# Optimization experiments

Measured on AMD Instinct MI355X. Metric: run time of the kernel, lower is better.

## Reference

```python
import math
import jax, jax.numpy as jnp
import numpy as np

NUM_HEADS = 16
QUERY_SIZE = 1024
SEQ = 2048
HEAD = QUERY_SIZE // NUM_HEADS  # qk_size = vo_size = 64


def setup_inputs() -> dict:
    key = jax.random.key(0)
    ks = jax.random.split(key, 8)
    s = 0.02
    query = jax.random.normal(ks[0], (SEQ, QUERY_SIZE), jnp.float32)
    key_ = jax.random.normal(ks[1], (SEQ, QUERY_SIZE), jnp.float32)
    value = jax.random.normal(ks[2], (SEQ, QUERY_SIZE), jnp.float32)
    # causal mask (mask='causal' with state=None -> offset 0)
    mask = jnp.tril(jnp.ones((SEQ, SEQ), dtype=bool))
    Wq = jax.random.normal(ks[3], (QUERY_SIZE, QUERY_SIZE), jnp.float32) * s
    Wk = jax.random.normal(ks[4], (QUERY_SIZE, QUERY_SIZE), jnp.float32) * s
    Wv = jax.random.normal(ks[5], (QUERY_SIZE, QUERY_SIZE), jnp.float32) * s
    Wo = jax.random.normal(ks[6], (QUERY_SIZE, QUERY_SIZE), jnp.float32) * s
    return {"query": query, "key_": key_, "value": value, "mask": mask,
            "Wq": Wq, "Wk": Wk, "Wv": Wv, "Wo": Wo}


def reference(query, key_, value, mask, Wq, Wk, Wv, Wo):
    H, D = NUMS = NUM_HEADS, HEAD
    S = query.shape[0]
    inv_sqrt_d = 1.0 / math.sqrt(D)
    # per-token linear projections, split into heads: [S, H, D]
    q = (query @ Wq.T).reshape(S, H, D)
    k = (key_ @ Wk.T).reshape(S, H, D)
    v = (value @ Wv.T).reshape(S, H, D)
    # NOTE: original divides BOTH q and k by sqrt(d) (effective 1/d scaling)
    q = q * inv_sqrt_d
    k = k * inv_sqrt_d
    # logits per head: [H, S, S]
    logits = jnp.einsum('shd,Shd->hsS', q, k)
    logits = jnp.where(mask[None, :, :], logits, jnp.finfo(logits.dtype).min)
    # per-head GLOBAL max subtraction, softmax in fp32, cast back (faithful)
    m = jnp.max(logits, axis=(1, 2), keepdims=True)
    weights = jax.nn.softmax((logits - m).astype(jnp.float32), axis=-1).astype(query.dtype)
    attn = jnp.einsum('hsS,ShD->shD', weights, v).reshape(S, H * D)
    return attn @ Wo.T
```

## Files before the change

### kernel.cpp

```cpp
#include <hip/hip_runtime.h>
#include <hip/hip_bf16.h>

typedef __bf16 bf16_t;
typedef __bf16 bf16x8 __attribute__((ext_vector_type(8)));
typedef float f32x4 __attribute__((ext_vector_type(4)));

#define MFMA(A, B, C) __builtin_amdgcn_mfma_f32_16x16x32_bf16(A, B, C, 0, 0, 0)

__global__ __launch_bounds__(256) void cvt_all(
    const float* __restrict__ q, const float* __restrict__ k, const float* __restrict__ v,
    const float* __restrict__ wq, const float* __restrict__ wk,
    const float* __restrict__ wv, const float* __restrict__ wo,
    bf16_t* __restrict__ xq, bf16_t* __restrict__ xk, bf16_t* __restrict__ xv,
    bf16_t* __restrict__ ywq, bf16_t* __restrict__ ywk,
    bf16_t* __restrict__ ywv, bf16_t* __restrict__ ywo)
{
  const long gid = (long)blockIdx.x * 256 + threadIdx.x;
  const float* s; bf16_t* d; long off; float sc = 1.0f;
  if (gid < 262144)       { s = q;  d = xq;  off = gid; }
  else if (gid < 524288)  { s = k;  d = xk;  off = gid - 262144; }
  else if (gid < 786432)  { s = v;  d = xv;  off = gid - 524288; }
  else if (gid < 917504)  { s = wq; d = ywq; off = gid - 786432;  sc = 0.125f; }
  else if (gid < 1048576) { s = wk; d = ywk; off = gid - 917504;  sc = 0.125f; }
  else if (gid < 1179648) { s = wv; d = ywv; off = gid - 1048576; }
  else                    { s = wo; d = ywo; off = gid - 1179648; }
  const float* p = s + off * 8;
  float4 a = *(const float4*)p, b = *(const float4*)(p + 4);
  bf16x8 o;
  o[0] = (bf16_t)(a.x * sc); o[1] = (bf16_t)(a.y * sc);
  o[2] = (bf16_t)(a.z * sc); o[3] = (bf16_t)(a.w * sc);
  o[4] = (bf16_t)(b.x * sc); o[5] = (bf16_t)(b.y * sc);
  o[6] = (bf16_t)(b.z * sc); o[7] = (bf16_t)(b.w * sc);
  *(bf16x8*)(d + off * 8) = o;
}

__device__ __forceinline__ void gemm_core(const bf16_t* __restrict__ A,
                                          const bf16_t* __restrict__ W,
                                          int bm, int bn,
                                          bf16_t* As, bf16_t* Bs,
                                          f32x4 (&acc)[4][2])
{
  const int tid = threadIdx.x, lane = tid & 63, wave = tid >> 6;
  const int l15 = lane & 15, l4 = lane >> 4;
  const int wm = (wave >> 1) * 64, wn = (wave & 1) * 32;

  bf16x8 ra[4], rb[2];
#pragma unroll
  for (int i = 0; i < 4; ++i) {
    int id = tid + 256 * i, row = id >> 3, c = id & 7;
    ra[i] = *(const bf16x8*)(A + (size_t)(bm + row) * 1024 + c * 8);
  }
#pragma unroll
  for (int i = 0; i < 2; ++i) {
    int id = tid + 256 * i, row = id >> 3, c = id & 7;
    rb[i] = *(const bf16x8*)(W + (size_t)(bn + row) * 1024 + c * 8);
  }

#pragma unroll
  for (int s = 0; s < 16; ++s) {
    __syncthreads();
#pragma unroll
    for (int i = 0; i < 4; ++i) {
      int id = tid + 256 * i, row = id >> 3, c = id & 7;
      *(bf16x8*)(&As[row * 64 + 8 * (c ^ (row & 7))]) = ra[i];
    }
#pragma unroll
    for (int i = 0; i < 2; ++i) {
      int id = tid + 256 * i, row = id >> 3, c = id & 7;
      *(bf16x8*)(&Bs[row * 64 + 8 * (c ^ (row & 7))]) = rb[i];
    }
    __syncthreads();
    if (s + 1 < 16) {
      const int k0 = (s + 1) * 64;
#pragma unroll
      for (int i = 0; i < 4; ++i) {
        int id = tid + 256 * i, row = id >> 3, c = id & 7;
        ra[i] = *(const bf16x8*)(A + (size_t)(bm + row) * 1024 + k0 + c * 8);
      }
#pragma unroll
      for (int i = 0; i < 2; ++i) {
        int id = tid + 256 * i, row = id >> 3, c = id & 7;
        rb[i] = *(const bf16x8*)(W + (size_t)(bn + row) * 1024 + k0 + c * 8);
      }
    }
#pragma unroll
    for (int ks = 0; ks < 2; ++ks) {
      bf16x8 af[4], bfr[2];
#pragma unroll
      for (int i = 0; i < 4; ++i)
        af[i] = *(const bf16x8*)(&As[(wm + i * 16 + l15) * 64 + 8 * ((ks * 4 + l4) ^ (l15 & 7))]);
#pragma unroll
      for (int j = 0; j < 2; ++j)
        bfr[j] = *(const bf16x8*)(&Bs[(wn + j * 16 + l15) * 64 + 8 * ((ks * 4 + l4) ^ (l15 & 7))]);
#pragma unroll
      for (int i = 0; i < 4; ++i)
#pragma unroll
        for (int j = 0; j < 2; ++j)
          acc[i][j] = MFMA(af[i], bfr[j], acc[i][j]);
    }
  }
}

__global__ __launch_bounds__(256) void gemm_qkv(
    const bf16_t* __restrict__ xq, const bf16_t* __restrict__ xk, const bf16_t* __restrict__ xv,
    const bf16_t* __restrict__ ywq, const bf16_t* __restrict__ ywk, const bf16_t* __restrict__ ywv,
    bf16_t* __restrict__ qo, bf16_t* __restrict__ ko, bf16_t* __restrict__ vt)
{
  __shared__ __align__(16) bf16_t As[128 * 64];
  __shared__ __align__(16) bf16_t Bs[64 * 64];
  const int z = blockIdx.z;
  const bf16_t* A = z == 0 ? xq : z == 1 ? xk : xv;
  const bf16_t* W = z == 0 ? ywq : z == 1 ? ywk : ywv;
  const int bm = blockIdx.x * 128, bn = blockIdx.y * 64;
  f32x4 acc[4][2] = {};
  gemm_core(A, W, bm, bn, As, Bs, acc);
  const int tid = threadIdx.x, lane = tid & 63, wave = tid >> 6;
  const int l15 = lane & 15, l4 = lane >> 4;
  const int wm = (wave >> 1) * 64, wn = (wave & 1) * 32;
  if (z < 2) {
    bf16_t* C = z == 0 ? qo : ko;
#pragma unroll
    for (int i = 0; i < 4; ++i)
#pragma unroll
      for (int j = 0; j < 2; ++j)
#pragma unroll
        for (int r = 0; r < 4; ++r)
          C[(size_t)(bm + wm + i * 16 + 4 * l4 + r) * 1024 + bn + wn + j * 16 + l15] =
              (bf16_t)acc[i][j][r];
  } else {
#pragma unroll
    for (int i = 0; i < 4; ++i)
#pragma unroll
      for (int j = 0; j < 2; ++j)
#pragma unroll
        for (int r = 0; r < 4; ++r)
          vt[(size_t)(bn + wn + j * 16 + l15) * 2048 + bm + wm + i * 16 + 4 * l4 + r] =
              (bf16_t)acc[i][j][r];
  }
}

__global__ __launch_bounds__(256) void gemm_out(
    const bf16_t* __restrict__ ctx, const bf16_t* __restrict__ ywo, float* __restrict__ out)
{
  __shared__ __align__(16) bf16_t As[128 * 64];
  __shared__ __align__(16) bf16_t Bs[64 * 64];
  const int bm = blockIdx.x * 128, bn = blockIdx.y * 64;
  f32x4 acc[4][2] = {};
  gemm_core(ctx, ywo, bm, bn, As, Bs, acc);
  const int tid = threadIdx.x, lane = tid & 63, wave = tid >> 6;
  const int l15 = lane & 15, l4 = lane >> 4;
  const int wm = (wave >> 1) * 64, wn = (wave & 1) * 32;
#pragma unroll
  for (int i = 0; i < 4; ++i)
#pragma unroll
    for (int j = 0; j < 2; ++j)
#pragma unroll
      for (int r = 0; r < 4; ++r)
        out[(size_t)(bm + wm + i * 16 + 4 * l4 + r) * 1024 + bn + wn + j * 16 + l15] =
            acc[i][j][r];
}

__global__ __launch_bounds__(256) void attn256(
    const bf16_t* __restrict__ Qb, const bf16_t* __restrict__ Kb,
    const bf16_t* __restrict__ Vt, bf16_t* __restrict__ Ctx)
{
  __shared__ __align__(16) bf16_t Ks[2][64 * 64];
  __shared__ __align__(16) bf16_t Vs[2][64 * 64];
  __shared__ __align__(16) bf16_t Ps[4][16 * 64];
  const int h = blockIdx.x >> 4, j0 = blockIdx.x & 15;
  const int hoff = h * 64;
  const int tid = threadIdx.x, lane = tid & 63, wave = tid >> 6;
  const int l15 = lane & 15, l4 = lane >> 4;

  for (int job = 0; job < 2; ++job) {
    const int qt = job ? (31 - j0) : j0;
    const int qb = qt * 64;
    const int nch = qt + 1;
    const int qrow = qb + wave * 16 + l15;
    bf16x8 qf0 = *(const bf16x8*)(Qb + (size_t)qrow * 1024 + hoff + 8 * l4);
    bf16x8 qf1 = *(const bf16x8*)(Qb + (size_t)qrow * 1024 + hoff + 32 + 8 * l4);
    f32x4 oacc[4] = {};
    float den[4] = {0.f, 0.f, 0.f, 0.f};

    {
      bf16x8 rk[2], rv[2];
#pragma unroll
      for (int i = 0; i < 2; ++i) {
        int id = tid + 256 * i, r = id >> 3, c = id & 7;
        rk[i] = *(const bf16x8*)(Kb + (size_t)r * 1024 + hoff + c * 8);
        rv[i] = *(const bf16x8*)(Vt + (size_t)(hoff + r) * 2048 + c * 8);
      }
      __syncthreads();
#pragma unroll
      for (int i = 0; i < 2; ++i) {
        int id = tid + 256 * i, r = id >> 3, c = id & 7;
        *(bf16x8*)(&Ks[0][r * 64 + 8 * (c ^ (r & 7))]) = rk[i];
        *(bf16x8*)(&Vs[0][r * 64 + 8 * (c ^ (r & 7))]) = rv[i];
      }
    }
    int cur = 0;
    for (int c = 0; c < nch; ++c) {
      bf16x8 rk[2], rv[2];
      const bool pre = (c + 1 < nch);
      if (pre) {
        const int t0n = (c + 1) * 64;
#pragma unroll
        for (int i = 0; i < 2; ++i) {
          int id = tid + 256 * i, r = id >> 3, cc = id & 7;
          rk[i] = *(const bf16x8*)(Kb + (size_t)(t0n + r) * 1024 + hoff + cc * 8);
          rv[i] = *(const bf16x8*)(Vt + (size_t)(hoff + r) * 2048 + t0n + cc * 8);
        }
      }
      __syncthreads();
      const int t0 = c * 64;
#pragma unroll
      for (int sub = 0; sub < 4; ++sub) {
        bf16x8 kf0 = *(const bf16x8*)(&Ks[cur][(sub * 16 + l15) * 64 + 8 * ((l4) ^ (l15 & 7))]);
        bf16x8 kf1 = *(const bf16x8*)(&Ks[cur][(sub * 16 + l15) * 64 + 8 * ((4 + l4) ^ (l15 & 7))]);
        f32x4 sv = {};
        sv = MFMA(qf0, kf0, sv);
        sv = MFMA(qf1, kf1, sv);
        const int t = t0 + sub * 16 + l15;
#pragma unroll
        for (int r = 0; r < 4; ++r) {
          const int qq = qb + wave * 16 + 4 * l4 + r;
          const float p = (t <= qq) ? __expf(sv[r]) : 0.0f;
          const bf16_t pb = (bf16_t)p;
          den[r] += (float)pb;
          const int row = 4 * l4 + r;
          const int ch = sub * 2 + (l15 >> 3);
          Ps[wave][row * 64 + 8 * (ch ^ (row & 7)) + (l15 & 7)] = pb;
        }
      }
      asm volatile("s_waitcnt lgkmcnt(0)" ::: "memory");
#pragma unroll
      for (int ks = 0; ks < 2; ++ks) {
        bf16x8 pf = *(const bf16x8*)(&Ps[wave][l15 * 64 + 8 * ((ks * 4 + l4) ^ (l15 & 7))]);
#pragma unroll
        for (int db = 0; db < 4; ++db) {
          bf16x8 vf = *(const bf16x8*)(&Vs[cur][(db * 16 + l15) * 64 + 8 * ((ks * 4 + l4) ^ (l15 & 7))]);
          oacc[db] = MFMA(pf, vf, oacc[db]);
        }
      }
      if (pre) {
#pragma unroll
        for (int i = 0; i < 2; ++i) {
          int id = tid + 256 * i, r = id >> 3, cc = id & 7;
          *(bf16x8*)(&Ks[cur ^ 1][r * 64 + 8 * (cc ^ (r & 7))]) = rk[i];
          *(bf16x8*)(&Vs[cur ^ 1][r * 64 + 8 * (cc ^ (r & 7))]) = rv[i];
        }
      }
      cur ^= 1;
    }
#pragma unroll
    for (int r = 0; r < 4; ++r)
#pragma unroll
      for (int m = 1; m < 16; m <<= 1)
        den[r] += __shfl_xor(den[r], m, 64);
#pragma unroll
    for (int r = 0; r < 4; ++r) {
      const int qq = qb + wave * 16 + 4 * l4 + r;
      const float inv = 1.0f / den[r];
#pragma unroll
      for (int db = 0; db < 4; ++db)
        Ctx[(size_t)qq * 1024 + hoff + db * 16 + l15] = (bf16_t)(oacc[db][r] * inv);
    }
  }
}

extern "C" void kernel_launch(void* const* d_in, const int* in_sizes, int n_in,
                              void* d_out, int out_size, void* d_ws, size_t ws_size,
                              hipStream_t stream)
{
  const float* query = (const float*)d_in[0];
  const float* key_  = (const float*)d_in[1];
  const float* value = (const float*)d_in[2];
  const float* Wq = (const float*)d_in[4];
  const float* Wk = (const float*)d_in[5];
  const float* Wv = (const float*)d_in[6];
  const float* Wo = (const float*)d_in[7];
  float* out = (float*)d_out;

  const size_t SE = (size_t)2048 * 1024, EE = (size_t)1024 * 1024;
  bf16_t* xq  = (bf16_t*)d_ws;
  bf16_t* xk  = xq + SE;
  bf16_t* xv  = xk + SE;
  bf16_t* wq  = xv + SE;
  bf16_t* wk  = wq + EE;
  bf16_t* wv  = wk + EE;
  bf16_t* wo  = wv + EE;
  bf16_t* qo  = wo + EE;
  bf16_t* ko  = qo + SE;
  bf16_t* vt  = ko + SE;
  bf16_t* ctx = vt + SE;

  cvt_all<<<5120, 256, 0, stream>>>(query, key_, value, Wq, Wk, Wv, Wo,
                                    xq, xk, xv, wq, wk, wv, wo);
  gemm_qkv<<<dim3(16, 16, 3), 256, 0, stream>>>(xq, xk, xv, wq, wk, wv, qo, ko, vt);
  attn256<<<256, 256, 0, stream>>>(qo, ko, vt, ctx);
  gemm_out<<<dim3(16, 16), 256, 0, stream>>>(ctx, wo, out);
}
```

Before: 86.73 us.

## Split attention KV chunks across two wave groups and process paired query tiles together

The attention kernel grows from 256 to 512 threads. Two groups of four waves each take one half of a 128-key chunk, and both paired causal query tiles (jp and 31-jp) are processed in one pass over shared K/V instead of two separate passes. Partial outputs and denominators from the second wave group are merged through shared memory at the end, and heads are remapped across blocks. The intent is to halve K/V loads per pair and add more waves for latency hiding. The cost is more shared memory, a final reduction step and some idle waves on the causal boundary.

```diff
diff --git a/kernel.cpp b/kernel.cpp
--- a/kernel.cpp
+++ b/kernel.cpp
@@ -160,110 +160,145 @@
             acc[i][j][r];
 }
 
-__global__ __launch_bounds__(256) void attn256(
+__global__ __launch_bounds__(512) void attn512(
     const bf16_t* __restrict__ Qb, const bf16_t* __restrict__ Kb,
     const bf16_t* __restrict__ Vt, bf16_t* __restrict__ Ctx)
 {
-  __shared__ __align__(16) bf16_t Ks[2][64 * 64];
-  __shared__ __align__(16) bf16_t Vs[2][64 * 64];
-  __shared__ __align__(16) bf16_t Ps[4][16 * 64];
-  const int h = blockIdx.x >> 4, j0 = blockIdx.x & 15;
+  __shared__ __align__(16) bf16_t Ks[2][128 * 64];
+  __shared__ __align__(16) bf16_t Vs[2][64 * 128];
+  __shared__ __align__(16) bf16_t Ps[8][16 * 64];
+
+  const int bid = blockIdx.x;
+  const int h = 2 * (bid & 7) + ((bid >> 3) >> 4);
+  const int jp = (bid >> 3) & 15;
   const int hoff = h * 64;
-  const int tid = threadIdx.x, lane = tid & 63, wave = tid >> 6;
+  const int tid = threadIdx.x;
+  const int lane = tid & 63, wave = tid >> 6;
+  const int g = wave & 3, kh = wave >> 2;
   const int l15 = lane & 15, l4 = lane >> 4;
-
-  for (int job = 0; job < 2; ++job) {
-    const int qt = job ? (31 - j0) : j0;
-    const int qb = qt * 64;
-    const int nch = qt + 1;
-    const int qrow = qb + wave * 16 + l15;
-    bf16x8 qf0 = *(const bf16x8*)(Qb + (size_t)qrow * 1024 + hoff + 8 * l4);
-    bf16x8 qf1 = *(const bf16x8*)(Qb + (size_t)qrow * 1024 + hoff + 32 + 8 * l4);
-    f32x4 oacc[4] = {};
-    float den[4] = {0.f, 0.f, 0.f, 0.f};
-
-    {
-      bf16x8 rk[2], rv[2];
-#pragma unroll
-      for (int i = 0; i < 2; ++i) {
-        int id = tid + 256 * i, r = id >> 3, c = id & 7;
-        rk[i] = *(const bf16x8*)(Kb + (size_t)r * 1024 + hoff + c * 8);
-        rv[i] = *(const bf16x8*)(Vt + (size_t)(hoff + r) * 2048 + c * 8);
-      }
-      __syncthreads();
-#pragma unroll
-      for (int i = 0; i < 2; ++i) {
-        int id = tid + 256 * i, r = id >> 3, c = id & 7;
-        *(bf16x8*)(&Ks[0][r * 64 + 8 * (c ^ (r & 7))]) = rk[i];
-        *(bf16x8*)(&Vs[0][r * 64 + 8 * (c ^ (r & 7))]) = rv[i];
-      }
-    }
-    int cur = 0;
-    for (int c = 0; c < nch; ++c) {
-      bf16x8 rk[2], rv[2];
-      const bool pre = (c + 1 < nch);
-      if (pre) {
-        const int t0n = (c + 1) * 64;
-#pragma unroll
-        for (int i = 0; i < 2; ++i) {
-          int id = tid + 256 * i, r = id >> 3, cc = id & 7;
-          rk[i] = *(const bf16x8*)(Kb + (size_t)(t0n + r) * 1024 + hoff + cc * 8);
-          rv[i] = *(const bf16x8*)(Vt + (size_t)(hoff + r) * 2048 + t0n + cc * 8);
-        }
-      }
-      __syncthreads();
-      const int t0 = c * 64;
-#pragma unroll
-      for (int sub = 0; sub < 4; ++sub) {
-        bf16x8 kf0 = *(const bf16x8*)(&Ks[cur][(sub * 16 + l15) * 64 + 8 * ((l4) ^ (l15 & 7))]);
-        bf16x8 kf1 = *(const bf16x8*)(&Ks[cur][(sub * 16 + l15) * 64 + 8 * ((4 + l4) ^ (l15 & 7))]);
-        f32x4 sv = {};
-        sv = MFMA(qf0, kf0, sv);
-        sv = MFMA(qf1, kf1, sv);
-        const int t = t0 + sub * 16 + l15;
-#pragma unroll
-        for (int r = 0; r < 4; ++r) {
-          const int qq = qb + wave * 16 + 4 * l4 + r;
-          const float p = (t <= qq) ? __expf(sv[r]) : 0.0f;
-          const bf16_t pb = (bf16_t)p;
-          den[r] += (float)pb;
-          const int row = 4 * l4 + r;
-          const int ch = sub * 2 + (l15 >> 3);
-          Ps[wave][row * 64 + 8 * (ch ^ (row & 7)) + (l15 & 7)] = pb;
-        }
-      }
-      asm volatile("s_waitcnt lgkmcnt(0)" ::: "memory");
-#pragma unroll
-      for (int ks = 0; ks < 2; ++ks) {
-        bf16x8 pf = *(const bf16x8*)(&Ps[wave][l15 * 64 + 8 * ((ks * 4 + l4) ^ (l15 & 7))]);
-#pragma unroll
-        for (int db = 0; db < 4; ++db) {
-          bf16x8 vf = *(const bf16x8*)(&Vs[cur][(db * 16 + l15) * 64 + 8 * ((ks * 4 + l4) ^ (l15 & 7))]);
-          oacc[db] = MFMA(pf, vf, oacc[db]);
-        }
-      }
-      if (pre) {
-#pragma unroll
-        for (int i = 0; i < 2; ++i) {
-          int id = tid + 256 * i, r = id >> 3, cc = id & 7;
-          *(bf16x8*)(&Ks[cur ^ 1][r * 64 + 8 * (cc ^ (r & 7))]) = rk[i];
-          *(bf16x8*)(&Vs[cur ^ 1][r * 64 + 8 * (cc ^ (r & 7))]) = rv[i];
-        }
-      }
-      cur ^= 1;
-    }
-#pragma unroll
-    for (int r = 0; r < 4; ++r)
-#pragma unroll
-      for (int m = 1; m < 16; m <<= 1)
-        den[r] += __shfl_xor(den[r], m, 64);
+  const int l7 = l15 & 7;
+
+  const int qtA = jp, qtB = 31 - jp;
+  const int qbA = qtA * 64, qbB = qtB * 64;
+  const int nscA = qtA / 2 + 1, nscB = qtB / 2 + 1;
+
+  const int qrA = qbA + g * 16 + l15, qrB = qbB + g * 16 + l15;
+  bf16x8 qA0 = *(const bf16x8*)(Qb + (size_t)qrA * 1024 + hoff + 8 * l4);
+  bf16x8 qA1 = *(const bf16x8*)(Qb + (size_t)qrA * 1024 + hoff + 32 + 8 * l4);
+  bf16x8 qB0 = *(const bf16x8*)(Qb + (size_t)qrB * 1024 + hoff + 8 * l4);
+  bf16x8 qB1 = *(const bf16x8*)(Qb + (size_t)qrB * 1024 + hoff + 32 + 8 * l4);
+
+  f32x4 oA[4] = {}, oB[4] = {};
+  float dA[4] = {0.f, 0.f, 0.f, 0.f}, dB[4] = {0.f, 0.f, 0.f, 0.f};
+
+  bf16x8 rk[2], rv[2];
+  auto issue = [&](int sc) {
+    const int t0 = sc * 128;
+#pragma unroll
+    for (int i = 0; i < 2; ++i) {
+      const int id = tid + 512 * i;
+      const int kr = id >> 3, kc = id & 7;
+      rk[i] = *(const bf16x8*)(Kb + (size_t)(t0 + kr) * 1024 + hoff + 8 * kc);
+      const int vr = id >> 4, vc = id & 15;
+      rv[i] = *(const bf16x8*)(Vt + (size_t)(hoff + vr) * 2048 + t0 + 8 * vc);
+    }
+  };
+  auto commit = [&](int buf) {
+#pragma unroll
+    for (int i = 0; i < 2; ++i) {
+      const int id = tid + 512 * i;
+      const int kr = id >> 3, kc = id & 7;
+      *(bf16x8*)(&Ks[buf][kr * 64 + 8 * (kc ^ (kr & 7))]) = rk[i];
+      const int vr = id >> 4, vc = id & 15;
+      *(bf16x8*)(&Vs[buf][vr * 128 + 8 * (vc ^ (vr & 7))]) = rv[i];
+    }
+  };
+
+  auto process = [&](int sc, int cur, int qb, const bf16x8& q0, const bf16x8& q1,
+                     f32x4 (&oacc)[4], float (&den)[4]) {
+    if (128 * sc + 64 * kh > qb + g * 16 + 15) return;
+    const int tb = 128 * sc + 64 * kh;
+#pragma unroll
+    for (int sub = 0; sub < 4; ++sub) {
+      const int krow = 64 * kh + 16 * sub + l15;
+      bf16x8 kf0 = *(const bf16x8*)(&Ks[cur][krow * 64 + 8 * (l4 ^ l7)]);
+      bf16x8 kf1 = *(const bf16x8*)(&Ks[cur][krow * 64 + 8 * ((4 + l4) ^ l7)]);
+      f32x4 sv = {};
+      sv = MFMA(q0, kf0, sv);
+      sv = MFMA(q1, kf1, sv);
+      const int t = tb + 16 * sub + l15;
+#pragma unroll
+      for (int r = 0; r < 4; ++r) {
+        const int qq = qb + g * 16 + 4 * l4 + r;
+        const float p = (t <= qq) ? __expf(sv[r]) : 0.0f;
+        const bf16_t pb = (bf16_t)p;
+        den[r] += (float)pb;
+        const int prow = 4 * l4 + r;
+        const int pch = 2 * sub + (l15 >> 3);
+        Ps[wave][prow * 64 + 8 * (pch ^ (prow & 7)) + l7] = pb;
+      }
+    }
+    asm volatile("s_waitcnt lgkmcnt(0)" ::: "memory");
+#pragma unroll
+    for (int ks = 0; ks < 2; ++ks) {
+      bf16x8 pf = *(const bf16x8*)(&Ps[wave][l15 * 64 + 8 * ((ks * 4 + l4) ^ l7)]);
+#pragma unroll
+      for (int db = 0; db < 4; ++db) {
+        bf16x8 vf = *(const bf16x8*)(&Vs[cur][(db * 16 + l15) * 128 + 64 * kh + 8 * ((ks * 4 + l4) ^ l7)]);
+        oacc[db] = MFMA(pf, vf, oacc[db]);
+      }
+    }
+  };
+
+  issue(0);
+  commit(0);
+  int cur = 0;
+  for (int sc = 0; sc < nscB; ++sc) {
+    const bool pre = (sc + 1 < nscB);
+    if (pre) issue(sc + 1);
+    __syncthreads();
+    process(sc, cur, qbB, qB0, qB1, oB, dB);
+    if (sc < nscA) process(sc, cur, qbA, qA0, qA1, oA, dA);
+    if (pre) commit(cur ^ 1);
+    cur ^= 1;
+  }
+
+  __syncthreads();
+#pragma unroll
+  for (int r = 0; r < 4; ++r)
+#pragma unroll
+    for (int m = 1; m < 16; m <<= 1) {
+      dA[r] += __shfl_xor(dA[r], m, 64);
+      dB[r] += __shfl_xor(dB[r], m, 64);
+    }
+  float* Os = (float*)(&Ks[0][0]);
+  float* Ds = (float*)(&Vs[0][0]);
+  if (kh == 1) {
 #pragma unroll
     for (int r = 0; r < 4; ++r) {
-      const int qq = qb + wave * 16 + 4 * l4 + r;
-      const float inv = 1.0f / den[r];
-#pragma unroll
-      for (int db = 0; db < 4; ++db)
-        Ctx[(size_t)qq * 1024 + hoff + db * 16 + l15] = (bf16_t)(oacc[db][r] * inv);
+      const int row = g * 16 + 4 * l4 + r;
+#pragma unroll
+      for (int db = 0; db < 4; ++db) {
+        Os[(0 * 64 + row) * 64 + db * 16 + l15] = oA[db][r];
+        Os[(1 * 64 + row) * 64 + db * 16 + l15] = oB[db][r];
+      }
+      if (l15 == 0) { Ds[0 * 64 + row] = dA[r]; Ds[1 * 64 + row] = dB[r]; }
+    }
+  }
+  __syncthreads();
+  if (kh == 0) {
+#pragma unroll
+    for (int r = 0; r < 4; ++r) {
+      const int row = g * 16 + 4 * l4 + r;
+      const float iA = 1.0f / (dA[r] + Ds[0 * 64 + row]);
+      const float iB = 1.0f / (dB[r] + Ds[1 * 64 + row]);
+#pragma unroll
+      for (int db = 0; db < 4; ++db) {
+        const float vA = oA[db][r] + Os[(0 * 64 + row) * 64 + db * 16 + l15];
+        const float vB = oB[db][r] + Os[(1 * 64 + row) * 64 + db * 16 + l15];
+        Ctx[(size_t)(qbA + row) * 1024 + hoff + db * 16 + l15] = (bf16_t)(vA * iA);
+        Ctx[(size_t)(qbB + row) * 1024 + hoff + db * 16 + l15] = (bf16_t)(vB * iB);
+      }
     }
   }
 }
@@ -297,6 +332,6 @@
   cvt_all<<<5120, 256, 0, stream>>>(query, key_, value, Wq, Wk, Wv, Wo,
                                     xq, xk, xv, wq, wk, wv, wo);
   gemm_qkv<<<dim3(16, 16, 3), 256, 0, stream>>>(xq, xk, xv, wq, wk, wv, qo, ko, vt);
-  attn256<<<256, 256, 0, stream>>>(qo, ko, vt, ctx);
+  attn512<<<256, 512, 0, stream>>>(qo, ko, vt, ctx);
   gemm_out<<<dim3(16, 16), 256, 0, stream>>>(ctx, wo, out);
 }
```

Measured after the change: 73.54 us. 1.18x faster.
